# Kernel tuning notes

Measured on AMD Instinct MI355X. Metric: run time of the kernel, lower is better.

## Reference

```python
import jax, jax.numpy as jnp
import numpy as np
from jax import lax

NPOINT, RADIUS, NSAMPLE = 512, 0.5, 32
MLP = [9, 64, 64, 128]
EPS = 1e-5


def setup_inputs() -> dict:
    key = jax.random.key(0)
    ks = jax.random.split(key, 2 + 2 * (len(MLP) - 1))
    inp = {
        "xyz": jax.random.normal(ks[0], (16, 3, 4096), jnp.float32),
        "features": jax.random.normal(ks[1], (16, 6, 4096), jnp.float32),
    }
    for i in range(len(MLP) - 1):
        cin, cout = MLP[i], MLP[i + 1]
        inp[f"W{i}"] = jax.random.normal(ks[2 + 2 * i], (cout, cin), jnp.float32) / np.sqrt(cin).astype(np.float32)
        inp[f"b{i}"] = jax.random.normal(ks[3 + 2 * i], (cout,), jnp.float32) * 0.01
        inp[f"g{i}"] = jnp.ones((cout,), jnp.float32)
        inp[f"beta{i}"] = jnp.zeros((cout,), jnp.float32)
    return inp


def farthest_point_sample(pts, npoint):
    # pts: [B, N, 3] -> idx [B, npoint]
    B, N, _ = pts.shape

    def step(carry, _):
        dist, far = carry  # dist [B,N], far [B]
        centroid = jnp.take_along_axis(pts, far[:, None, None], axis=1)  # [B,1,3]
        d = jnp.sum((pts - centroid) ** 2, axis=-1)
        dist = jnp.minimum(dist, d)
        return (dist, jnp.argmax(dist, axis=-1).astype(jnp.int32)), far

    init = (jnp.full((B, N), 1e10, pts.dtype), jnp.zeros((B,), jnp.int32))
    _, idx = lax.scan(step, init, None, length=npoint)
    return jnp.transpose(idx)  # [B, npoint]


def query_ball_point(radius, nsample, pts, new_xyz):
    # pts [B,N,3], new_xyz [B,K,3] -> idx [B,K,nsample]
    B, N, _ = pts.shape
    K = new_xyz.shape[1]
    sqrd = jnp.sum((new_xyz[:, :, None, :] - pts[:, None, :, :]) ** 2, axis=-1)  # [B,K,N]
    idx = jnp.broadcast_to(jnp.arange(N, dtype=jnp.int32), (B, K, N))
    idx = jnp.where(sqrd > radius * radius, N, idx)
    idx = jnp.sort(idx, axis=-1)[:, :, :nsample]
    first = idx[:, :, :1]  # centroid itself always within radius -> valid
    return jnp.where(idx == N, first, idx)


def _sa_forward(xyz, features, params):
    pts = jnp.transpose(xyz, (0, 2, 1))       # [B,N,3]
    feat = jnp.transpose(features, (0, 2, 1))  # [B,N,D]
    fps_idx = farthest_point_sample(pts, NPOINT)
    new_xyz = jnp.take_along_axis(pts, fps_idx[..., None], axis=1)  # [B,K,3]
    idx = query_ball_point(RADIUS, NSAMPLE, pts, new_xyz)            # [B,K,S]
    gather = jax.vmap(lambda p, i: p[i])
    grouped_xyz = gather(pts, idx) - new_xyz[:, :, None, :]          # [B,K,S,3]
    x = jnp.concatenate([grouped_xyz, gather(feat, idx)], axis=-1)   # [B,K,S,3+D]
    for (W, b, g, be) in params:
        x = jnp.einsum('bksc,oc->bkso', x, W) + b                    # 1x1 conv
        mu = jnp.mean(x, axis=(0, 1, 2))
        var = jnp.var(x, axis=(0, 1, 2))                             # BN train-mode stats
        x = jax.nn.relu((x - mu) * lax.rsqrt(var + EPS) * g + be)
    new_feat = jnp.max(x, axis=2)                                    # max over samples S
    return jnp.transpose(new_xyz, (0, 2, 1)), jnp.transpose(new_feat, (0, 2, 1))


def reference(xyz, features, W0, b0, g0, beta0, W1, b1, g1, beta1, W2, b2, g2, beta2):
    params = [(W0, b0, g0, beta0), (W1, b1, g1, beta1), (W2, b2, g2, beta2)]
    return _sa_forward(xyz, features, params)
```

## Files before the change

### kernel.cpp

```cpp
#include <hip/hip_runtime.h>
#include <cstdint>
#include <cstddef>

#define NPTS 4096
#define NP   512
#define NS   32
#define NB   16
#define NTOT (NB*NP*NS)
#define NBLK 1024

typedef float v2f __attribute__((ext_vector_type(2)));

__device__ __forceinline__ v2f pk_fma(v2f a, v2f b, v2f c) {
  v2f d;
  asm("v_pk_fma_f32 %0, %1, %2, %3" : "=v"(d) : "v"(a), "v"(b), "v"(c));
  return d;
}

template<int CTRL>
__device__ __forceinline__ float dpp_mov_f(float v) {
  return __int_as_float(__builtin_amdgcn_update_dpp(0, __float_as_int(v), CTRL, 0xf, 0xf, true));
}
template<int CTRL>
__device__ __forceinline__ unsigned dpp_mov_u(unsigned v) {
  return (unsigned)__builtin_amdgcn_update_dpp(0, (int)v, CTRL, 0xf, 0xf, true);
}
__device__ __forceinline__ float wave_sum_l63(float v) {
  v += dpp_mov_f<0x111>(v);
  v += dpp_mov_f<0x112>(v);
  v += dpp_mov_f<0x114>(v);
  v += dpp_mov_f<0x118>(v);
  v += dpp_mov_f<0x142>(v);
  v += dpp_mov_f<0x143>(v);
  return v;
}
__device__ __forceinline__ float wave_fmax_l63(float v) {
  v = fmaxf(v, dpp_mov_f<0x111>(v));
  v = fmaxf(v, dpp_mov_f<0x112>(v));
  v = fmaxf(v, dpp_mov_f<0x114>(v));
  v = fmaxf(v, dpp_mov_f<0x118>(v));
  v = fmaxf(v, dpp_mov_f<0x142>(v));
  v = fmaxf(v, dpp_mov_f<0x143>(v));
  return v;
}
__device__ __forceinline__ unsigned wave_umax_l63(unsigned v) {
  unsigned o;
  o = dpp_mov_u<0x111>(v); v = v > o ? v : o;
  o = dpp_mov_u<0x112>(v); v = v > o ? v : o;
  o = dpp_mov_u<0x114>(v); v = v > o ? v : o;
  o = dpp_mov_u<0x118>(v); v = v > o ? v : o;
  o = dpp_mov_u<0x142>(v); v = v > o ? v : o;
  o = dpp_mov_u<0x143>(v); v = v > o ? v : o;
  return v;
}
template<int CTRL, int RMASK>
__device__ __forceinline__ float dpp_fmax_o(float v) {
  int r = __builtin_amdgcn_update_dpp(__float_as_int(v), __float_as_int(v), CTRL, RMASK, 0xF, false);
  return fmaxf(v, __int_as_float(r));
}
__device__ __forceinline__ float half_max(float v) {
  v = dpp_fmax_o<0x111, 0xF>(v);
  v = dpp_fmax_o<0x112, 0xF>(v);
  v = dpp_fmax_o<0x114, 0xF>(v);
  v = dpp_fmax_o<0x118, 0xF>(v);
  v = dpp_fmax_o<0x142, 0xA>(v);
  return v;
}

__global__ __launch_bounds__(256) void fps_v20(const float* __restrict__ xyz,
    float* __restrict__ new_xyz, float* __restrict__ outx)
{
  const int b = blockIdx.x, t = threadIdx.x;
  const float* base = xyz + (size_t)b*3*NPTS;
  __shared__ float4 s_pts[NPTS];
  __shared__ float  s_v[2][4];
  __shared__ int    s_i[2][4];
  float px[16], py[16], pz[16], dist[16];
#pragma unroll
  for (int q = 0; q < 16; ++q) {
    const int p = t + q*256;
    px[q] = base[p]; py[q] = base[NPTS+p]; pz[q] = base[2*NPTS+p];
    s_pts[p] = make_float4(px[q], py[q], pz[q], 0.f);
    dist[q] = 1e10f;
  }
  __syncthreads();
  float cx = base[0], cy = base[NPTS], cz = base[2*NPTS];
  const int wv = t >> 6, lane = t & 63;
  for (int it = 0; it < NP; ++it) {
    if (t == 0) {
      float* nx = new_xyz + ((size_t)b*NP + it)*3;
      nx[0] = cx; nx[1] = cy; nx[2] = cz;
      float* o = outx + (size_t)b*3*NP + it;
      o[0] = cx; o[NP] = cy; o[2*NP] = cz;
    }
    float bv = -1.f; int bi = 0;
#pragma unroll
    for (int q = 0; q < 16; ++q) {
      float dx = __fsub_rn(px[q], cx);
      float dy = __fsub_rn(py[q], cy);
      float dz = __fsub_rn(pz[q], cz);
      float d  = __fadd_rn(__fadd_rn(__fmul_rn(dx,dx), __fmul_rn(dy,dy)), __fmul_rn(dz,dz));
      d = fminf(dist[q], d);
      dist[q] = d;
      if (d > bv) { bv = d; bi = t + q*256; }
    }
    float wm = wave_fmax_l63(bv);
    float wmax = __int_as_float(__builtin_amdgcn_readlane(__float_as_int(wm), 63));
    unsigned cand = (bv == wmax) ? ~(unsigned)bi : 0u;
    unsigned cm = wave_umax_l63(cand);
    int fi_w = (int)~(unsigned)__builtin_amdgcn_readlane((int)cm, 63);
    const int ib = it & 1;
    if (lane == 0) { s_v[ib][wv] = wmax; s_i[ib][wv] = fi_w; }
    __syncthreads();
    float fv = s_v[ib][0]; int fi = s_i[ib][0];
#pragma unroll
    for (int w = 1; w < 4; ++w) {
      float vv = s_v[ib][w]; int ii = s_i[ib][w];
      if (vv > fv || (vv == fv && ii < fi)) { fv = vv; fi = ii; }
    }
    float4 c4 = s_pts[fi];
    cx = c4.x; cy = c4.y; cz = c4.z;
  }
}

__global__ __launch_bounds__(256) void ballq_v20(const float* __restrict__ xyz,
    const float* __restrict__ new_xyz, int* __restrict__ nidx)
{
  const int wid  = (blockIdx.x*256 + threadIdx.x) >> 6;
  const int lane = threadIdx.x & 63;
  const int b = wid >> 9;
  const float* base = xyz + (size_t)b*3*NPTS;
  const float* c = new_xyz + (size_t)wid*3;
  float cx = c[0], cy = c[1], cz = c[2];
  int* xi = nidx + (size_t)wid*NS;
  int cnt = 0, first_j = 0;
  for (int jb = 0; jb < NPTS && cnt < NS; jb += 64) {
    int j = jb + lane;
    float dxv = __fsub_rn(base[j],        cx);
    float dyv = __fsub_rn(base[NPTS+j],   cy);
    float dzv = __fsub_rn(base[2*NPTS+j], cz);
    float d = __fadd_rn(__fadd_rn(__fmul_rn(dxv,dxv), __fmul_rn(dyv,dyv)), __fmul_rn(dzv,dzv));
    bool in = !(d > 0.25f);
    unsigned long long m = __ballot(in);
    int pos = cnt + __popcll(m & ((1ull<<lane)-1ull));
    if (in && pos < NS) xi[pos] = j;
    if (cnt == 0 && m) first_j = jb + __builtin_ctzll(m);
    cnt += __popcll(m);
  }
  int nv = cnt < NS ? cnt : NS;
  for (int s = nv + lane; s < NS; s += 64) xi[s] = first_j;
}

__device__ __forceinline__ void load_x0_v20(const float* __restrict__ xyz,
    const float* __restrict__ feat, const float* __restrict__ nxyz,
    const int* __restrict__ nidx, int p, float x[9])
{
  const int wid = p >> 5;
  const int b   = wid >> 9;
  const int j   = nidx[p];
  const float* base = xyz  + (size_t)b*3*NPTS;
  const float* fb   = feat + (size_t)b*6*NPTS;
  const float* c    = nxyz + (size_t)wid*3;
  x[0] = __fsub_rn(base[j],        c[0]);
  x[1] = __fsub_rn(base[NPTS+j],   c[1]);
  x[2] = __fsub_rn(base[2*NPTS+j], c[2]);
#pragma unroll
  for (int cc = 0; cc < 6; ++cc) x[3+cc] = fb[cc*NPTS + j];
}

__device__ __forceinline__ float l0_dot(const float* __restrict__ W0, const v2f xp[4],
                                        float x8, float bias, int o) {
  const float* wr = W0 + o*9;
  v2f acc2 = {bias, 0.f};
#pragma unroll
  for (int k = 0; k < 4; ++k) {
    v2f w; w[0] = wr[2*k]; w[1] = wr[2*k+1];
    acc2 = pk_fma(w, xp[k], acc2);
  }
  return acc2[0] + acc2[1] + wr[8]*x8;
}
__device__ __forceinline__ float l64_dot(const float* __restrict__ W, const v2f xp[32],
                                         float bias, int o) {
  const v2f* wr = reinterpret_cast<const v2f*>(W + o*64);
  v2f acc2 = {bias, 0.f};
#pragma unroll
  for (int k = 0; k < 32; ++k) acc2 = pk_fma(wr[k], xp[k], acc2);
  return acc2[0] + acc2[1];
}

__global__ __launch_bounds__(256) void statsA_v20(const float* __restrict__ xyz,
    const float* __restrict__ feat, const float* __restrict__ nxyz, const int* __restrict__ nidx,
    const float* __restrict__ W0, const float* __restrict__ b0, float* __restrict__ part)
{
  __shared__ float sS[4][64], sQ[4][64];
  const int t = threadIdx.x;
  const int p = blockIdx.x*256 + t;
  float x[9];
  load_x0_v20(xyz, feat, nxyz, nidx, p, x);
  v2f xp[4];
#pragma unroll
  for (int k = 0; k < 4; ++k) { xp[k][0] = x[2*k]; xp[k][1] = x[2*k+1]; }
  const int wv = t>>6, lane = t&63;
  for (int o = 0; o < 64; ++o) {
    float acc = l0_dot(W0, xp, x[8], b0[o], o);
    float s = wave_sum_l63(acc);
    float q = wave_sum_l63(acc*acc);
    if (lane == 63) { sS[wv][o] = s; sQ[wv][o] = q; }
  }
  __syncthreads();
  if (t < 64) {
    part[(size_t)blockIdx.x*256 + t]       = sS[0][t]+sS[1][t]+sS[2][t]+sS[3][t];
    part[(size_t)blockIdx.x*256 + 128 + t] = sQ[0][t]+sQ[1][t]+sQ[2][t]+sQ[3][t];
  }
}

__global__ __launch_bounds__(256) void fin1_v20(float* __restrict__ part)
{
  const int g = blockIdx.x, t = threadIdx.x;
  double S = 0.0;
  for (int r = 0; r < 16; ++r) S += (double)part[(size_t)(g*16 + r)*256 + t];
  part[(size_t)g*16*256 + t] = (float)S;
}

__global__ __launch_bounds__(128) void fin2_v20(const float* __restrict__ part,
    const float* __restrict__ g, const float* __restrict__ beta,
    float* __restrict__ stats, int C)
{
  const int t = threadIdx.x;
  double S = 0.0, Q = 0.0;
  for (int bk = 0; bk < 64; ++bk) {
    S += (double)part[(size_t)bk*4096 + t];
    Q += (double)part[(size_t)bk*4096 + 128 + t];
  }
  if (t < C) {
    const double invN = 1.0/(double)NTOT;
    double mean = S*invN;
    double var  = Q*invN - mean*mean;
    float sc    = g[t] / (float)sqrt(var + 1e-5);
    stats[t] = (float)mean; stats[C+t] = sc; stats[2*C+t] = beta[t];
  }
}

__global__ __launch_bounds__(256) void statsB_v20(const float* __restrict__ xyz,
    const float* __restrict__ feat, const float* __restrict__ nxyz, const int* __restrict__ nidx,
    const float* __restrict__ W0, const float* __restrict__ b0, const float* __restrict__ st0,
    const float* __restrict__ W1, const float* __restrict__ b1, float* __restrict__ part)
{
  __shared__ float sS[4][64], sQ[4][64];
  const int t = threadIdx.x;
  const int p = blockIdx.x*256 + t;
  float x[9];
  load_x0_v20(xyz, feat, nxyz, nidx, p, x);
  v2f xp[4];
#pragma unroll
  for (int k = 0; k < 4; ++k) { xp[k][0] = x[2*k]; xp[k][1] = x[2*k+1]; }
  v2f x1p[32];
  for (int o = 0; o < 64; ++o) {
    float acc = l0_dot(W0, xp, x[8], b0[o], o);
    float v = fmaxf((acc - st0[o])*st0[64+o] + st0[128+o], 0.f);
    x1p[o>>1][o&1] = v;
  }
  const int wv = t>>6, lane = t&63;
  for (int o = 0; o < 64; ++o) {
    float acc = l64_dot(W1, x1p, b1[o], o);
    float s = wave_sum_l63(acc);
    float qv = wave_sum_l63(acc*acc);
    if (lane == 63) { sS[wv][o] = s; sQ[wv][o] = qv; }
  }
  __syncthreads();
  if (t < 64) {
    part[(size_t)blockIdx.x*256 + t]       = sS[0][t]+sS[1][t]+sS[2][t]+sS[3][t];
    part[(size_t)blockIdx.x*256 + 128 + t] = sQ[0][t]+sQ[1][t]+sQ[2][t]+sQ[3][t];
  }
}

__global__ __launch_bounds__(256) void statsC_v20(const float* __restrict__ xyz,
    const float* __restrict__ feat, const float* __restrict__ nxyz, const int* __restrict__ nidx,
    const float* __restrict__ W0, const float* __restrict__ b0, const float* __restrict__ st0,
    const float* __restrict__ W1, const float* __restrict__ b1, const float* __restrict__ st1,
    const float* __restrict__ W2, const float* __restrict__ b2,
    float* __restrict__ part, float* __restrict__ outf_raw)
{
  __shared__ float sS[4][128], sQ[4][128];
  const int t = threadIdx.x;
  const int p = blockIdx.x*256 + t;
  float x[9];
  load_x0_v20(xyz, feat, nxyz, nidx, p, x);
  v2f xp[4];
#pragma unroll
  for (int k = 0; k < 4; ++k) { xp[k][0] = x[2*k]; xp[k][1] = x[2*k+1]; }
  v2f x1p[32];
  for (int o = 0; o < 64; ++o) {
    float acc = l0_dot(W0, xp, x[8], b0[o], o);
    float v = fmaxf((acc - st0[o])*st0[64+o] + st0[128+o], 0.f);
    x1p[o>>1][o&1] = v;
  }
  v2f x2p[32];
  for (int o = 0; o < 64; ++o) {
    float acc = l64_dot(W1, x1p, b1[o], o);
    float v = fmaxf((acc - st1[o])*st1[64+o] + st1[128+o], 0.f);
    x2p[o>>1][o&1] = v;
  }
  const int wv = t>>6, lane = t&63;
  const int c  = p >> 5;
  for (int o = 0; o < 128; ++o) {
    float acc = l64_dot(W2, x2p, b2[o], o);
    float s = wave_sum_l63(acc);
    float qv = wave_sum_l63(acc*acc);
    if (lane == 63) { sS[wv][o] = s; sQ[wv][o] = qv; }
    float m = half_max(acc);
    if ((lane & 31) == 31)
      outf_raw[(size_t)(c>>9)*65536 + (size_t)o*512 + (c&511)] = m;
  }
  __syncthreads();
  if (t < 128) {
    part[(size_t)blockIdx.x*256 + t]       = sS[0][t]+sS[1][t]+sS[2][t]+sS[3][t];
    part[(size_t)blockIdx.x*256 + 128 + t] = sQ[0][t]+sQ[1][t]+sQ[2][t]+sQ[3][t];
  }
}

__global__ __launch_bounds__(256) void final_v20(float* __restrict__ outf,
    const float* __restrict__ st2)
{
  const int i = blockIdx.x*256 + threadIdx.x;
  const int o = (i >> 9) & 127;
  float v = outf[i];
  outf[i] = fmaxf((v - st2[o])*st2[128+o] + st2[256+o], 0.f);
}

extern "C" void kernel_launch(void* const* d_in, const int* in_sizes, int n_in,
                              void* d_out, int out_size, void* d_ws, size_t ws_size,
                              hipStream_t stream)
{
  const float* xyz = (const float*)d_in[0];
  const float* feat= (const float*)d_in[1];
  const float* W0  = (const float*)d_in[2];
  const float* b0  = (const float*)d_in[3];
  const float* g0  = (const float*)d_in[4];
  const float* be0 = (const float*)d_in[5];
  const float* W1  = (const float*)d_in[6];
  const float* b1  = (const float*)d_in[7];
  const float* g1  = (const float*)d_in[8];
  const float* be1 = (const float*)d_in[9];
  const float* W2  = (const float*)d_in[10];
  const float* b2  = (const float*)d_in[11];
  const float* g2  = (const float*)d_in[12];
  const float* be2 = (const float*)d_in[13];

  char* ws = (char*)d_ws;
  float* nxyz = (float*)(ws);
  int*   nidx = (int*)  (ws + 98304);
  float* part = (float*)(ws + 1146880);
  float* st0  = (float*)(ws + 2195456);
  float* st1  = (float*)(ws + 2196480);
  float* st2  = (float*)(ws + 2197504);

  float* outx = (float*)d_out;
  float* outf = outx + (size_t)16*3*512;

  fps_v20   <<<16,   256, 0, stream>>>(xyz, nxyz, outx);
  ballq_v20 <<<2048, 256, 0, stream>>>(xyz, nxyz, nidx);
  statsA_v20<<<NBLK, 256, 0, stream>>>(xyz, feat, nxyz, nidx, W0, b0, part);
  fin1_v20  <<<64,   256, 0, stream>>>(part);
  fin2_v20  <<<1,    128, 0, stream>>>(part, g0, be0, st0, 64);
  statsB_v20<<<NBLK, 256, 0, stream>>>(xyz, feat, nxyz, nidx, W0, b0, st0, W1, b1, part);
  fin1_v20  <<<64,   256, 0, stream>>>(part);
  fin2_v20  <<<1,    128, 0, stream>>>(part, g1, be1, st1, 64);
  statsC_v20<<<NBLK, 256, 0, stream>>>(xyz, feat, nxyz, nidx, W0, b0, st0, W1, b1, st1, W2, b2, part, outf);
  fin1_v20  <<<64,   256, 0, stream>>>(part);
  fin2_v20  <<<1,    128, 0, stream>>>(part, g2, be2, st2, 128);
  final_v20 <<<4096, 256, 0, stream>>>(outf, st2);
}
```

Measured before the change: 811.0 us.

## Parallelize ball query across a block with ballot masks and a prefix scan

```diff
diff --git a/kernel.cpp b/kernel.cpp
--- a/kernel.cpp
+++ b/kernel.cpp
@@ -24,6 +24,10 @@
 template<int CTRL>
 __device__ __forceinline__ unsigned dpp_mov_u(unsigned v) {
   return (unsigned)__builtin_amdgcn_update_dpp(0, (int)v, CTRL, 0xf, 0xf, true);
+}
+template<int CTRL, int RMASK>
+__device__ __forceinline__ int dpp_mov_i_rm(int v) {
+  return __builtin_amdgcn_update_dpp(0, v, CTRL, RMASK, 0xf, true);
 }
 __device__ __forceinline__ float wave_sum_l63(float v) {
   v += dpp_mov_f<0x111>(v);
@@ -53,6 +57,15 @@
   o = dpp_mov_u<0x143>(v); v = v > o ? v : o;
   return v;
 }
+__device__ __forceinline__ int wave_incl_scan(int v) {
+  v += dpp_mov_i_rm<0x111, 0xF>(v);
+  v += dpp_mov_i_rm<0x112, 0xF>(v);
+  v += dpp_mov_i_rm<0x114, 0xF>(v);
+  v += dpp_mov_i_rm<0x118, 0xF>(v);
+  v += dpp_mov_i_rm<0x142, 0xA>(v);
+  v += dpp_mov_i_rm<0x143, 0xC>(v);
+  return v;
+}
 template<int CTRL, int RMASK>
 __device__ __forceinline__ float dpp_fmax_o(float v) {
   int r = __builtin_amdgcn_update_dpp(__float_as_int(v), __float_as_int(v), CTRL, RMASK, 0xF, false);
@@ -67,7 +80,7 @@
   return v;
 }
 
-__global__ __launch_bounds__(256) void fps_v20(const float* __restrict__ xyz,
+__global__ __launch_bounds__(256) void fps_v21(const float* __restrict__ xyz,
     float* __restrict__ new_xyz, float* __restrict__ outx)
 {
   const int b = blockIdx.x, t = threadIdx.x;
@@ -123,35 +136,57 @@
   }
 }
 
-__global__ __launch_bounds__(256) void ballq_v20(const float* __restrict__ xyz,
+__global__ __launch_bounds__(256) void ballq_v21(const float* __restrict__ xyz,
     const float* __restrict__ new_xyz, int* __restrict__ nidx)
 {
-  const int wid  = (blockIdx.x*256 + threadIdx.x) >> 6;
-  const int lane = threadIdx.x & 63;
+  const int wid = blockIdx.x;
+  const int t = threadIdx.x, wv = t >> 6, lane = t & 63;
   const int b = wid >> 9;
   const float* base = xyz + (size_t)b*3*NPTS;
   const float* c = new_xyz + (size_t)wid*3;
-  float cx = c[0], cy = c[1], cz = c[2];
+  const float cx = c[0], cy = c[1], cz = c[2];
+  __shared__ unsigned long long s_mask[64];
+  __shared__ int s_excl[64];
+  __shared__ int s_first, s_nv;
   int* xi = nidx + (size_t)wid*NS;
-  int cnt = 0, first_j = 0;
-  for (int jb = 0; jb < NPTS && cnt < NS; jb += 64) {
-    int j = jb + lane;
+#pragma unroll
+  for (int k = 0; k < 16; ++k) {
+    const int ch = wv*16 + k;
+    const int j  = ch*64 + lane;
     float dxv = __fsub_rn(base[j],        cx);
     float dyv = __fsub_rn(base[NPTS+j],   cy);
     float dzv = __fsub_rn(base[2*NPTS+j], cz);
     float d = __fadd_rn(__fadd_rn(__fmul_rn(dxv,dxv), __fmul_rn(dyv,dyv)), __fmul_rn(dzv,dzv));
     bool in = !(d > 0.25f);
     unsigned long long m = __ballot(in);
-    int pos = cnt + __popcll(m & ((1ull<<lane)-1ull));
-    if (in && pos < NS) xi[pos] = j;
-    if (cnt == 0 && m) first_j = jb + __builtin_ctzll(m);
-    cnt += __popcll(m);
-  }
-  int nv = cnt < NS ? cnt : NS;
-  for (int s = nv + lane; s < NS; s += 64) xi[s] = first_j;
-}
-
-__device__ __forceinline__ void load_x0_v20(const float* __restrict__ xyz,
+    if (lane == 0) s_mask[ch] = m;
+  }
+  __syncthreads();
+  if (t < 64) {
+    unsigned long long m = s_mask[t];
+    int pc = __popcll(m);
+    int incl = wave_incl_scan(pc);
+    s_excl[t] = incl - pc;
+    unsigned long long chunkmask = __ballot(pc > 0);
+    int total = __builtin_amdgcn_readlane(incl, 63);
+    if (t == 0) {
+      int fc = __builtin_ctzll(chunkmask);
+      s_first = fc*64 + __builtin_ctzll(s_mask[fc]);
+      s_nv = total < NS ? total : NS;
+    }
+  }
+  __syncthreads();
+#pragma unroll
+  for (int k = 0; k < 16; ++k) {
+    const int ch = wv*16 + k;
+    unsigned long long m = s_mask[ch];
+    int pos = s_excl[ch] + __popcll(m & ((1ull << lane) - 1ull));
+    if (((m >> lane) & 1ull) && pos < NS) xi[pos] = ch*64 + lane;
+  }
+  if (t < NS && t >= s_nv) xi[t] = s_first;
+}
+
+__device__ __forceinline__ void load_x0_v21(const float* __restrict__ xyz,
     const float* __restrict__ feat, const float* __restrict__ nxyz,
     const int* __restrict__ nidx, int p, float x[9])
 {
@@ -188,7 +223,7 @@
   return acc2[0] + acc2[1];
 }
 
-__global__ __launch_bounds__(256) void statsA_v20(const float* __restrict__ xyz,
+__global__ __launch_bounds__(256) void statsA_v21(const float* __restrict__ xyz,
     const float* __restrict__ feat, const float* __restrict__ nxyz, const int* __restrict__ nidx,
     const float* __restrict__ W0, const float* __restrict__ b0, float* __restrict__ part)
 {
@@ -196,7 +231,7 @@
   const int t = threadIdx.x;
   const int p = blockIdx.x*256 + t;
   float x[9];
-  load_x0_v20(xyz, feat, nxyz, nidx, p, x);
+  load_x0_v21(xyz, feat, nxyz, nidx, p, x);
   v2f xp[4];
 #pragma unroll
   for (int k = 0; k < 4; ++k) { xp[k][0] = x[2*k]; xp[k][1] = x[2*k+1]; }
@@ -214,7 +249,7 @@
   }
 }
 
-__global__ __launch_bounds__(256) void fin1_v20(float* __restrict__ part)
+__global__ __launch_bounds__(256) void fin1_v21(float* __restrict__ part)
 {
   const int g = blockIdx.x, t = threadIdx.x;
   double S = 0.0;
@@ -222,7 +257,7 @@
   part[(size_t)g*16*256 + t] = (float)S;
 }
 
-__global__ __launch_bounds__(128) void fin2_v20(const float* __restrict__ part,
+__global__ __launch_bounds__(128) void fin2_v21(const float* __restrict__ part,
     const float* __restrict__ g, const float* __restrict__ beta,
     float* __restrict__ stats, int C)
 {
@@ -241,7 +276,7 @@
   }
 }
 
-__global__ __launch_bounds__(256) void statsB_v20(const float* __restrict__ xyz,
+__global__ __launch_bounds__(256) void statsB_v21(const float* __restrict__ xyz,
     const float* __restrict__ feat, const float* __restrict__ nxyz, const int* __restrict__ nidx,
     const float* __restrict__ W0, const float* __restrict__ b0, const float* __restrict__ st0,
     const float* __restrict__ W1, const float* __restrict__ b1, float* __restrict__ part)
@@ -250,7 +285,7 @@
   const int t = threadIdx.x;
   const int p = blockIdx.x*256 + t;
   float x[9];
-  load_x0_v20(xyz, feat, nxyz, nidx, p, x);
+  load_x0_v21(xyz, feat, nxyz, nidx, p, x);
   v2f xp[4];
 #pragma unroll
   for (int k = 0; k < 4; ++k) { xp[k][0] = x[2*k]; xp[k][1] = x[2*k+1]; }
@@ -274,7 +309,7 @@
   }
 }
 
-__global__ __launch_bounds__(256) void statsC_v20(const float* __restrict__ xyz,
+__global__ __launch_bounds__(256) void statsC_v21(const float* __restrict__ xyz,
     const float* __restrict__ feat, const float* __restrict__ nxyz, const int* __restrict__ nidx,
     const float* __restrict__ W0, const float* __restrict__ b0, const float* __restrict__ st0,
     const float* __restrict__ W1, const float* __restrict__ b1, const float* __restrict__ st1,
@@ -285,7 +320,7 @@
   const int t = threadIdx.x;
   const int p = blockIdx.x*256 + t;
   float x[9];
-  load_x0_v20(xyz, feat, nxyz, nidx, p, x);
+  load_x0_v21(xyz, feat, nxyz, nidx, p, x);
   v2f xp[4];
 #pragma unroll
   for (int k = 0; k < 4; ++k) { xp[k][0] = x[2*k]; xp[k][1] = x[2*k+1]; }
@@ -319,7 +354,7 @@
   }
 }
 
-__global__ __launch_bounds__(256) void final_v20(float* __restrict__ outf,
+__global__ __launch_bounds__(256) void final_v21(float* __restrict__ outf,
     const float* __restrict__ st2)
 {
   const int i = blockIdx.x*256 + threadIdx.x;
@@ -358,16 +393,16 @@
   float* outx = (float*)d_out;
   float* outf = outx + (size_t)16*3*512;
 
-  fps_v20   <<<16,   256, 0, stream>>>(xyz, nxyz, outx);
-  ballq_v20 <<<2048, 256, 0, stream>>>(xyz, nxyz, nidx);
-  statsA_v20<<<NBLK, 256, 0, stream>>>(xyz, feat, nxyz, nidx, W0, b0, part);
-  fin1_v20  <<<64,   256, 0, stream>>>(part);
-  fin2_v20  <<<1,    128, 0, stream>>>(part, g0, be0, st0, 64);
-  statsB_v20<<<NBLK, 256, 0, stream>>>(xyz, feat, nxyz, nidx, W0, b0, st0, W1, b1, part);
-  fin1_v20  <<<64,   256, 0, stream>>>(part);
-  fin2_v20  <<<1,    128, 0, stream>>>(part, g1, be1, st1, 64);
-  statsC_v20<<<NBLK, 256, 0, stream>>>(xyz, feat, nxyz, nidx, W0, b0, st0, W1, b1, st1, W2, b2, part, outf);
-  fin1_v20  <<<64,   256, 0, stream>>>(part);
-  fin2_v20  <<<1,    128, 0, stream>>>(part, g2, be2, st2, 128);
-  final_v20 <<<4096, 256, 0, stream>>>(outf, st2);
-}
+  fps_v21   <<<16,   256, 0, stream>>>(xyz, nxyz, outx);
+  ballq_v21 <<<8192, 256, 0, stream>>>(xyz, nxyz, nidx);
+  statsA_v21<<<NBLK, 256, 0, stream>>>(xyz, feat, nxyz, nidx, W0, b0, part);
+  fin1_v21  <<<64,   256, 0, stream>>>(part);
+  fin2_v21  <<<1,    128, 0, stream>>>(part, g0, be0, st0, 64);
+  statsB_v21<<<NBLK, 256, 0, stream>>>(xyz, feat, nxyz, nidx, W0, b0, st0, W1, b1, part);
+  fin1_v21  <<<64,   256, 0, stream>>>(part);
+  fin2_v21  <<<1,    128, 0, stream>>>(part, g1, be1, st1, 64);
+  statsC_v21<<<NBLK, 256, 0, stream>>>(xyz, feat, nxyz, nidx, W0, b0, st0, W1, b1, st1, W2, b2, part, outf);
+  fin1_v21  <<<64,   256, 0, stream>>>(part);
+  fin2_v21  <<<1,    128, 0, stream>>>(part, g2, be2, st2, 128);
+  final_v21 <<<4096, 256, 0, stream>>>(outf, st2);
+}
```

New measurement: 811.1 us. About the same (+0.0%).
